# Kernel optimization log

Measured on AMD Instinct MI355X. Metric: run time of the kernel, lower is better.

Reference implementation:

```python
import jax, jax.numpy as jnp
import numpy as np

BETA = 0.001  # init kwarg beta
S, K = 32768, 32  # segments x candidates-per-segment (uniform segments)


def setup_inputs() -> dict:
    key = jax.random.key(0)
    logits = jax.random.normal(key, (S * K,), dtype=jnp.float32)
    # cumulative segment offsets: [0, K, 2K, ..., S*K]  (uniform ragged structure)
    k_lens = jnp.arange(S + 1, dtype=jnp.int32) * K
    return {"logits": logits, "k_lens": k_lens}


def reference(logits, k_lens):
    # Static shapes derived from array shapes (uniform segments).
    n_seg = k_lens.shape[0] - 1              # S
    seg_len = logits.shape[0] // n_seg       # K
    seg = logits.reshape(n_seg, seg_len)     # [S, K]
    # torch.combinations(arange(K), 2) == upper-triangular index pairs (i < j)
    i_idx, j_idx = jnp.triu_indices(seg_len, k=1)  # each [P], P = K*(K-1)/2
    pos = seg[:, i_idx]                      # [S, P]
    neg = seg[:, j_idx]                      # [S, P]
    l2 = 0.5 * (pos * pos - neg * neg)
    # per-segment loss: -mean(logsigmoid(pos-neg) + beta*l2)
    loss = -jnp.mean(jax.nn.log_sigmoid(pos - neg) + BETA * l2, axis=1)  # [S]
    return loss  # reduction=None -> stacked per-segment losses
```

## Files before the change

kernel.cpp:

```cpp
#include <hip/hip_runtime.h>


struct PairTab { unsigned short v[64][8]; };
constexpr PairTab make_tab() {
    PairTab t{};
    unsigned short tmp[512] = {};
    int p = 0;
    for (int i = 0; i < 32; ++i)
        for (int j = i + 1; j < 32; ++j)
            tmp[p++] = (unsigned short)((i * 4) | ((j * 4) << 8));
    for (; p < 512; ++p) tmp[p] = 0;
    for (int it = 0; it < 8; ++it)
        for (int lane = 0; lane < 64; ++lane)
            t.v[lane][it] = tmp[it * 64 + lane];
    return t;
}
__constant__ PairTab TAB = make_tab();

__device__ __forceinline__ float bperm(int byteaddr, float v) {
    return __int_as_float(__builtin_amdgcn_ds_bpermute(byteaddr, __float_as_int(v)));
}

#if __has_builtin(__builtin_amdgcn_exp2f)
#define FAST_EXP2(x) __builtin_amdgcn_exp2f(x)
#else
#define FAST_EXP2(x) exp2f(x)
#endif
#if __has_builtin(__builtin_amdgcn_logf)
#define FAST_LOG2(x) __builtin_amdgcn_logf(x)
#else
#define FAST_LOG2(x) log2f(x)
#endif

__global__ __launch_bounds__(256) void rmloss_kernel(
        const float* __restrict__ logits, float* __restrict__ out, int n_seg) {
    const int lane = threadIdx.x & 63;
    const int seg  = blockIdx.x * 4 + (threadIdx.x >> 6);
    if (seg >= n_seg) return;

    float x = 0.0f;
    if (lane < 32) x = logits[(size_t)seg * 32 + lane];

    const uint4 tw = *reinterpret_cast<const uint4*>(&TAB.v[lane][0]);
    const unsigned int wds[4] = {tw.x, tw.y, tw.z, tw.w};

    constexpr float LOG2E = 1.4426950408889634f;
    constexpr float LN2   = 0.6931471805599453f;

    float acc = 0.0f;
#pragma unroll
    for (int it = 0; it < 8; ++it) {
        const unsigned int w  = wds[it >> 1];
        const unsigned int pk = (it & 1) ? (w >> 16) : (w & 0xffffu);
        const int ai = (int)(pk & 0xffu);
        const int aj = (int)((pk >> 8) & 0xffu);
        const float xi = bperm(ai, x);
        const float xj = bperm(aj, x);
        const float t  = xi - xj;
        const float e  = FAST_EXP2(t * -LOG2E);
        acc += FAST_LOG2(1.0f + e);
    }

    const float c = (float)(31 - 2 * lane);
    float r = LN2 * acc - 0.0005f * c * x * x;

#pragma unroll
    for (int off = 32; off; off >>= 1) r += __shfl_xor(r, off, 64);

    if (lane == 0) out[seg] = (r - 16.0f * LN2) * (1.0f / 496.0f);
}

extern "C" void kernel_launch(void* const* d_in, const int* in_sizes, int n_in,
                              void* d_out, int out_size, void* d_ws, size_t ws_size,
                              hipStream_t stream) {
    const float* logits = (const float*)d_in[0];
    const int n_seg = in_sizes[1] - 1;
    float* out = (float*)d_out;
    const int blocks = (n_seg + 3) / 4;
    rmloss_kernel<<<blocks, 256, 0, stream>>>(logits, out, n_seg);
}
```

Baseline: 63.01 us.

## Pack two segments per wavefront and premultiply logits by log2e

Each 64-lane wavefront now handles two 32-element segments, one per half-wave, using a rebuilt permute table that offsets the second half by 128 bytes. This removes the idle half-wave lanes and the padded dummy pairs of the old layout, at the cost of 16 pair iterations per lane instead of 8. The logits are scaled by log2e once before the loop, which drops a multiply per pair. Blocks grow to 1024 threads covering 32 segments, the final reduction runs only within each half-wave, and the padding correction is applied per lane.

```diff
diff --git a/kernel.cpp b/kernel.cpp
--- a/kernel.cpp
+++ b/kernel.cpp
@@ -1,21 +1,33 @@
 #include <hip/hip_runtime.h>
 
 
-struct PairTab { unsigned short v[64][8]; };
-constexpr PairTab make_tab() {
-    PairTab t{};
-    unsigned short tmp[512] = {};
+constexpr int K = 32;
+constexpr int ITERS = 16;
+
+struct alignas(16) Tab {
+    unsigned int A[64][4];
+    unsigned int B[64][4];
+};
+constexpr Tab make_tab() {
+    Tab t{};
+    unsigned char ai[512] = {}, aj[512] = {};
     int p = 0;
-    for (int i = 0; i < 32; ++i)
-        for (int j = i + 1; j < 32; ++j)
-            tmp[p++] = (unsigned short)((i * 4) | ((j * 4) << 8));
-    for (; p < 512; ++p) tmp[p] = 0;
-    for (int it = 0; it < 8; ++it)
-        for (int lane = 0; lane < 64; ++lane)
-            t.v[lane][it] = tmp[it * 64 + lane];
+    for (int i = 0; i < K; ++i)
+        for (int j = i + 1; j < K; ++j) { ai[p] = (unsigned char)(i * 4); aj[p] = (unsigned char)(j * 4); ++p; }
+    for (int it = 0; it < ITERS; ++it)
+        for (int l = 0; l < 32; ++l) {
+            const int s = it * 32 + l;
+            for (int half = 0; half < 2; ++half) {
+                const int lane = l + 32 * half;
+                const unsigned int a = ai[s] + 128u * half;
+                const unsigned int b = aj[s] + 128u * half;
+                t.A[lane][it >> 2] |= a << ((it & 3) * 8);
+                t.B[lane][it >> 2] |= b << ((it & 3) * 8);
+            }
+        }
     return t;
 }
-__constant__ PairTab TAB = make_tab();
+__constant__ Tab TAB = make_tab();
 
 __device__ __forceinline__ float bperm(int byteaddr, float v) {
     return __int_as_float(__builtin_amdgcn_ds_bpermute(byteaddr, __float_as_int(v)));
@@ -32,42 +44,47 @@
 #define FAST_LOG2(x) log2f(x)
 #endif
 
-__global__ __launch_bounds__(256) void rmloss_kernel(
+__global__ __launch_bounds__(1024) void rmloss_kernel(
         const float* __restrict__ logits, float* __restrict__ out, int n_seg) {
     const int lane = threadIdx.x & 63;
-    const int seg  = blockIdx.x * 4 + (threadIdx.x >> 6);
-    if (seg >= n_seg) return;
+    const int wave = blockIdx.x * 16 + (threadIdx.x >> 6);
+    const int seg0 = wave * 2;
+    if (seg0 >= n_seg) return;
 
+    const long long gidx = (long long)wave * 64 + lane;
     float x = 0.0f;
-    if (lane < 32) x = logits[(size_t)seg * 32 + lane];
-
-    const uint4 tw = *reinterpret_cast<const uint4*>(&TAB.v[lane][0]);
-    const unsigned int wds[4] = {tw.x, tw.y, tw.z, tw.w};
+    if (gidx < (long long)n_seg * K) x = logits[gidx];
 
     constexpr float LOG2E = 1.4426950408889634f;
     constexpr float LN2   = 0.6931471805599453f;
+    const float y = x * LOG2E;
+
+    const uint4 wa = *reinterpret_cast<const uint4*>(&TAB.A[lane][0]);
+    const uint4 wb = *reinterpret_cast<const uint4*>(&TAB.B[lane][0]);
+    const unsigned int Aw[4] = {wa.x, wa.y, wa.z, wa.w};
+    const unsigned int Bw[4] = {wb.x, wb.y, wb.z, wb.w};
 
     float acc = 0.0f;
 #pragma unroll
-    for (int it = 0; it < 8; ++it) {
-        const unsigned int w  = wds[it >> 1];
-        const unsigned int pk = (it & 1) ? (w >> 16) : (w & 0xffffu);
-        const int ai = (int)(pk & 0xffu);
-        const int aj = (int)((pk >> 8) & 0xffu);
-        const float xi = bperm(ai, x);
-        const float xj = bperm(aj, x);
-        const float t  = xi - xj;
-        const float e  = FAST_EXP2(t * -LOG2E);
-        acc += FAST_LOG2(1.0f + e);
+    for (int it = 0; it < ITERS; ++it) {
+        const int w = it >> 2, sh = (it & 3) * 8;
+        const int ai = (int)((Aw[w] >> sh) & 0xffu);
+        const int aj = (int)((Bw[w] >> sh) & 0xffu);
+        const float yi = bperm(ai, y);
+        const float yj = bperm(aj, y);
+        acc += FAST_LOG2(1.0f + FAST_EXP2(yj - yi));
     }
 
-    const float c = (float)(31 - 2 * lane);
-    float r = LN2 * acc - 0.0005f * c * x * x;
+    const int k = lane & 31;
+    float r = LN2 * (acc - 0.5f) - 0.0005f * (float)(31 - 2 * k) * x * x;
 
 #pragma unroll
-    for (int off = 32; off; off >>= 1) r += __shfl_xor(r, off, 64);
+    for (int off = 16; off; off >>= 1) r += __shfl_xor(r, off, 64);
 
-    if (lane == 0) out[seg] = (r - 16.0f * LN2) * (1.0f / 496.0f);
+    if ((lane & 31) == 0) {
+        const int seg = seg0 + (lane >> 5);
+        if (seg < n_seg) out[seg] = r * (1.0f / 496.0f);
+    }
 }
 
 extern "C" void kernel_launch(void* const* d_in, const int* in_sizes, int n_in,
@@ -76,6 +93,7 @@
     const float* logits = (const float*)d_in[0];
     const int n_seg = in_sizes[1] - 1;
     float* out = (float*)d_out;
-    const int blocks = (n_seg + 3) / 4;
-    rmloss_kernel<<<blocks, 256, 0, stream>>>(logits, out, n_seg);
+    const int segs_per_block = 32;
+    const int blocks = (n_seg + segs_per_block - 1) / segs_per_block;
+    rmloss_kernel<<<blocks, 1024, 0, stream>>>(logits, out, n_seg);
 }
```

Result: no change. 61.83 us (-1.9%).
